# Kernel optimization log

Hardware: AMD Instinct MI355X
Metric: run time of the kernel (lower is better)

## Reference

```python
import jax, jax.numpy as jnp
import numpy as np

N_ROW, N_COL, RANK = 8192, 8192, 256

def setup_inputs() -> dict:
    key = jax.random.key(0)
    k1, k2, k3 = jax.random.split(key, 3)
    X = jax.random.normal(k1, (N_ROW, RANK), dtype=jnp.float32)
    Y = jax.random.normal(k2, (RANK, N_COL), dtype=jnp.float32)
    beta = jax.random.normal(k3, (1,), dtype=jnp.float32)
    return {"X": X, "Y": Y, "beta": beta}

def reference(X, Y, beta):
    # mathematically equal to torch.norm(X[:,None] - Y.T, dim=-1).
    x2 = jnp.sum(X * X, axis=1, keepdims=True)          # (n_row, 1)
    y2 = jnp.sum(Y * Y, axis=0, keepdims=True)          # (1, n_col)
    cross = X @ Y                                        # (n_row, n_col) GEMM
    d2 = jnp.maximum(x2 + y2 - 2.0 * cross, 0.0)
    norms = jnp.sqrt(d2)
    z = -norms + beta                                    # beta broadcasts (1,)
    return z
```

## Files before the change

kernel.cpp:

```cpp
#include <hip/hip_runtime.h>

#define NROW 8192
#define NCOL 8192
#define RANK 256

#define BM 128
#define BN 128
#define BK 64
#define NKT (RANK / BK)

typedef __bf16  bf16x8 __attribute__((ext_vector_type(8)));
typedef float   f32x4  __attribute__((ext_vector_type(4)));

__device__ __forceinline__ unsigned short f2bf(float f) {
    unsigned int u = __builtin_bit_cast(unsigned int, f);
    u += 0x7fffu + ((u >> 16) & 1u);
    return (unsigned short)(u >> 16);
}

__global__ __launch_bounds__(256) void prep_x(const float* __restrict__ X,
                                              unsigned short* __restrict__ Xb,
                                              float* __restrict__ x2) {
    const int row  = blockIdx.x * 4 + (threadIdx.x >> 6);
    const int lane = threadIdx.x & 63;
    const float4 v = ((const float4*)(X + (size_t)row * RANK))[lane];
    float s = v.x * v.x + v.y * v.y + v.z * v.z + v.w * v.w;
    ushort4 b;
    b.x = f2bf(v.x); b.y = f2bf(v.y); b.z = f2bf(v.z); b.w = f2bf(v.w);
    ((ushort4*)(Xb + (size_t)row * RANK))[lane] = b;
    #pragma unroll
    for (int off = 32; off > 0; off >>= 1) s += __shfl_down(s, off);
    if (lane == 0) x2[row] = s;
}

__global__ __launch_bounds__(256) void prep_y(const float* __restrict__ Y,
                                              unsigned short* __restrict__ Ybt,
                                              float* __restrict__ y2) {
    __shared__ float tile[64][65];
    __shared__ float part[256];
    const int t  = threadIdx.x;
    const int j0 = blockIdx.x * 64;
    const int tq = t >> 6;
    const int tl = t & 63;
    float acc = 0.f;
    for (int c = 0; c < 4; ++c) {
        const int k0 = c * 64;
        #pragma unroll
        for (int i = 0; i < 16; ++i) {
            const int kk = tq * 16 + i;
            const float v = Y[(size_t)(k0 + kk) * NCOL + j0 + tl];
            tile[kk][tl] = v;
            acc += v * v;
        }
        __syncthreads();
        #pragma unroll
        for (int i = 0; i < 16; ++i) {
            const int jj = tq * 16 + i;
            Ybt[(size_t)(j0 + jj) * RANK + k0 + tl] = f2bf(tile[tl][jj]);
        }
        __syncthreads();
    }
    part[t] = acc;
    __syncthreads();
    if (t < 64)
        y2[j0 + t] = part[t] + part[t + 64] + part[t + 128] + part[t + 192];
}

__global__ __launch_bounds__(256, 2)
void l2_gemm(const unsigned short* __restrict__ A,
             const unsigned short* __restrict__ Bt,
             const float* __restrict__ x2,
             const float* __restrict__ y2,
             const float* __restrict__ beta_p,
             float* __restrict__ out) {
    __shared__ alignas(16) unsigned short As[2][BM * BK];
    __shared__ alignas(16) unsigned short Bs[2][BN * BK];

    const int t    = threadIdx.x;
    const int wid  = t >> 6;
    const int lane = t & 63;

    const int bid  = blockIdx.x;
    const int xcd  = bid & 7;
    const int seq  = bid >> 3;
    const int ct   = xcd * 8 + (seq & 7);
    const int rt   = seq >> 3;
    const int rowBase = rt * BM;
    const int colBase = ct * BN;

    const int waveM = (wid >> 1) * 64;
    const int waveN = (wid & 1) * 64;

    f32x4 acc[4][4] = {};

    const int lrow = lane >> 3;
    const int lcol = (lane & 7) * 8;

    const unsigned short* gA = A  + (size_t)(rowBase + wid * 8 + lrow) * RANK + lcol;
    const unsigned short* gB = Bt + (size_t)(colBase + wid * 8 + lrow) * RANK + lcol;

    auto stage = [&](int buf, int kt) {
        #pragma unroll
        for (int r = 0; r < 4; ++r) {
            const int rrel = r * 32 + wid * 8;
            __builtin_amdgcn_global_load_lds(
                (__attribute__((address_space(1))) void*)(gA + (size_t)r * 32 * RANK + kt),
                (__attribute__((address_space(3))) void*)(&As[buf][rrel * BK]), 16, 0, 0);
            __builtin_amdgcn_global_load_lds(
                (__attribute__((address_space(1))) void*)(gB + (size_t)r * 32 * RANK + kt),
                (__attribute__((address_space(3))) void*)(&Bs[buf][rrel * BK]), 16, 0, 0);
        }
    };

    auto compute = [&](int buf) {
        #pragma unroll
        for (int ks = 0; ks < BK; ks += 32) {
            const int kfrag = ks + (lane >> 4) * 8;
            bf16x8 af[4], bfr[4];
            #pragma unroll
            for (int mt = 0; mt < 4; ++mt)
                af[mt] = *(const bf16x8*)(&As[buf][(waveM + mt * 16 + (lane & 15)) * BK + kfrag]);
            #pragma unroll
            for (int nt = 0; nt < 4; ++nt)
                bfr[nt] = *(const bf16x8*)(&Bs[buf][(waveN + nt * 16 + (lane & 15)) * BK + kfrag]);
            #pragma unroll
            for (int mt = 0; mt < 4; ++mt)
                #pragma unroll
                for (int nt = 0; nt < 4; ++nt)
                    acc[mt][nt] = __builtin_amdgcn_mfma_f32_16x16x32_bf16(
                        bfr[nt], af[mt], acc[mt][nt], 0, 0, 0);
        }
    };

    stage(0, 0);
    __syncthreads();
    #pragma unroll
    for (int kt = 1; kt < NKT; ++kt) {
        stage(kt & 1, kt * BK);
        compute((kt - 1) & 1);
        __syncthreads();
    }

    const int r0 = rowBase + waveM + (lane & 15);
    const int c0 = colBase + waveN + ((lane >> 4) << 2);
    const float beta = *beta_p;
    float xv[4];
    f32x4 y4[4];
    #pragma unroll
    for (int mt = 0; mt < 4; ++mt) xv[mt] = x2[r0 + mt * 16];
    #pragma unroll
    for (int nt = 0; nt < 4; ++nt) y4[nt] = *(const f32x4*)(y2 + c0 + nt * 16);

    compute((NKT - 1) & 1);

    #pragma unroll
    for (int mt = 0; mt < 4; ++mt) {
        const int row = r0 + mt * 16;
        float* op = out + (size_t)row * NCOL + c0;
        #pragma unroll
        for (int nt = 0; nt < 4; ++nt) {
            const f32x4 a = acc[mt][nt];
            f32x4 z;
            #pragma unroll
            for (int r = 0; r < 4; ++r) {
                float d2 = xv[mt] + y4[nt][r] - 2.0f * a[r];
                z[r] = beta - __builtin_amdgcn_sqrtf(fmaxf(d2, 0.0f));
            }
            __builtin_nontemporal_store(z, (f32x4*)(op + nt * 16));
        }
    }
}

extern "C" void kernel_launch(void* const* d_in, const int* in_sizes, int n_in,
                              void* d_out, int out_size, void* d_ws, size_t ws_size,
                              hipStream_t stream) {
    const float* X    = (const float*)d_in[0];
    const float* Y    = (const float*)d_in[1];
    const float* beta = (const float*)d_in[2];
    float* out = (float*)d_out;

    char* ws = (char*)d_ws;
    unsigned short* Xb  = (unsigned short*)(ws);
    unsigned short* Ybt = (unsigned short*)(ws + (size_t)4 * 1024 * 1024);
    float* x2 = (float*)(ws + (size_t)8 * 1024 * 1024);
    float* y2 = (float*)(ws + (size_t)8 * 1024 * 1024 + 32 * 1024);

    prep_x<<<NROW / 4, 256, 0, stream>>>(X, Xb, x2);
    prep_y<<<NCOL / 64, 256, 0, stream>>>(Y, Ybt, y2);

    l2_gemm<<<dim3(4096), 256, 0, stream>>>(Xb, Ybt, x2, y2, beta, out);
}
```

Baseline: 326.3 us.

## Stage full-K B tile in swizzled LDS, load A fragments directly from global

Replaces the double-buffered K-tiled LDS pipeline with one upfront load of the whole 128x256 B tile into LDS, using an XOR swizzle to avoid bank conflicts. The A operand fragments are now read straight from global memory into registers per k-group, and there is only a single barrier. This removes the per-iteration barriers and the LDS round trip for A. In exchange, A reads are per-lane 16-byte gathers from global memory that depend on cache hits, and nothing overlaps the global B load with compute.

```diff
diff --git a/kernel.cpp b/kernel.cpp
--- a/kernel.cpp
+++ b/kernel.cpp
@@ -6,8 +6,6 @@
 
 #define BM 128
 #define BN 128
-#define BK 64
-#define NKT (RANK / BK)
 
 typedef __bf16  bf16x8 __attribute__((ext_vector_type(8)));
 typedef float   f32x4  __attribute__((ext_vector_type(4)));
@@ -73,8 +71,7 @@
              const float* __restrict__ y2,
              const float* __restrict__ beta_p,
              float* __restrict__ out) {
-    __shared__ alignas(16) unsigned short As[2][BM * BK];
-    __shared__ alignas(16) unsigned short Bs[2][BN * BK];
+    __shared__ alignas(16) unsigned short Bs[BN * RANK];
 
     const int t    = threadIdx.x;
     const int wid  = t >> 6;
@@ -93,56 +90,31 @@
 
     f32x4 acc[4][4] = {};
 
-    const int lrow = lane >> 3;
-    const int lcol = (lane & 7) * 8;
-
-    const unsigned short* gA = A  + (size_t)(rowBase + wid * 8 + lrow) * RANK + lcol;
-    const unsigned short* gB = Bt + (size_t)(colBase + wid * 8 + lrow) * RANK + lcol;
-
-    auto stage = [&](int buf, int kt) {
+    {
+        const int l5 = lane >> 5;
+        const int ls = lane & 31;
         #pragma unroll
-        for (int r = 0; r < 4; ++r) {
-            const int rrel = r * 32 + wid * 8;
+        for (int r = 0; r < 16; ++r) {
+            const int ro = wid * 32 + r * 2 + l5;
+            const int cs = ls ^ (ro & 7);
+            const unsigned short* gp =
+                Bt + (size_t)(colBase + ro) * RANK + cs * 8;
+            unsigned short* lp = &Bs[(wid * 32 + r * 2) * RANK];
             __builtin_amdgcn_global_load_lds(
-                (__attribute__((address_space(1))) void*)(gA + (size_t)r * 32 * RANK + kt),
-                (__attribute__((address_space(3))) void*)(&As[buf][rrel * BK]), 16, 0, 0);
-            __builtin_amdgcn_global_load_lds(
-                (__attribute__((address_space(1))) void*)(gB + (size_t)r * 32 * RANK + kt),
-                (__attribute__((address_space(3))) void*)(&Bs[buf][rrel * BK]), 16, 0, 0);
+                (__attribute__((address_space(1))) void*)gp,
+                (__attribute__((address_space(3))) void*)lp, 16, 0, 0);
         }
-    };
-
-    auto compute = [&](int buf) {
-        #pragma unroll
-        for (int ks = 0; ks < BK; ks += 32) {
-            const int kfrag = ks + (lane >> 4) * 8;
-            bf16x8 af[4], bfr[4];
-            #pragma unroll
-            for (int mt = 0; mt < 4; ++mt)
-                af[mt] = *(const bf16x8*)(&As[buf][(waveM + mt * 16 + (lane & 15)) * BK + kfrag]);
-            #pragma unroll
-            for (int nt = 0; nt < 4; ++nt)
-                bfr[nt] = *(const bf16x8*)(&Bs[buf][(waveN + nt * 16 + (lane & 15)) * BK + kfrag]);
-            #pragma unroll
-            for (int mt = 0; mt < 4; ++mt)
-                #pragma unroll
-                for (int nt = 0; nt < 4; ++nt)
-                    acc[mt][nt] = __builtin_amdgcn_mfma_f32_16x16x32_bf16(
-                        bfr[nt], af[mt], acc[mt][nt], 0, 0, 0);
-        }
-    };
-
-    stage(0, 0);
-    __syncthreads();
-    #pragma unroll
-    for (int kt = 1; kt < NKT; ++kt) {
-        stage(kt & 1, kt * BK);
-        compute((kt - 1) & 1);
-        __syncthreads();
     }
 
     const int r0 = rowBase + waveM + (lane & 15);
     const int c0 = colBase + waveN + ((lane >> 4) << 2);
+    const int koff = (lane >> 4) * 8;
+
+    bf16x8 af0[4];
+    #pragma unroll
+    for (int mt = 0; mt < 4; ++mt)
+        af0[mt] = *(const bf16x8*)(A + (size_t)(r0 + mt * 16) * RANK + koff);
+
     const float beta = *beta_p;
     float xv[4];
     f32x4 y4[4];
@@ -151,7 +123,34 @@
     #pragma unroll
     for (int nt = 0; nt < 4; ++nt) y4[nt] = *(const f32x4*)(y2 + c0 + nt * 16);
 
-    compute((NKT - 1) & 1);
+    __syncthreads();
+
+    #pragma unroll
+    for (int kg = 0; kg < 8; ++kg) {
+        bf16x8 af[4], bfr[4];
+        if (kg == 0) {
+            #pragma unroll
+            for (int mt = 0; mt < 4; ++mt) af[mt] = af0[mt];
+        } else {
+            const int ko = kg * 32 + koff;
+            #pragma unroll
+            for (int mt = 0; mt < 4; ++mt)
+                af[mt] = *(const bf16x8*)(A + (size_t)(r0 + mt * 16) * RANK + ko);
+        }
+        const int sbase = kg * 4 + (lane >> 4);
+        #pragma unroll
+        for (int nt = 0; nt < 4; ++nt) {
+            const int rr = waveN + nt * 16 + (lane & 15);
+            const int s  = sbase ^ (rr & 7);
+            bfr[nt] = *(const bf16x8*)(&Bs[rr * RANK + s * 8]);
+        }
+        #pragma unroll
+        for (int mt = 0; mt < 4; ++mt)
+            #pragma unroll
+            for (int nt = 0; nt < 4; ++nt)
+                acc[mt][nt] = __builtin_amdgcn_mfma_f32_16x16x32_bf16(
+                    bfr[nt], af[mt], acc[mt][nt], 0, 0, 0);
+    }
 
     #pragma unroll
     for (int mt = 0; mt < 4; ++mt) {
```

Result: slower. 350.9 us (+7.5%).

## Stage GEMM epilogue through swizzled LDS for coalesced row stores; simplify grid mapping

Applied to the files above, without the earlier changes.

The epilogue now writes results into a shared-memory tile using an XOR swizzle, then reads them back so that each half-wave stores a full 512-byte contiguous row segment to global memory. The goal is better-coalesced writes of the 256 MB output, which is the dominant cost. The XCD-aware block remapping is replaced by a plain 2D grid, and nontemporal stores become regular stores. This adds two barriers and an LDS round trip, and may lose L2 locality across XCDs.

```diff
diff --git a/kernel.cpp b/kernel.cpp
--- a/kernel.cpp
+++ b/kernel.cpp
@@ -73,20 +73,16 @@
              const float* __restrict__ y2,
              const float* __restrict__ beta_p,
              float* __restrict__ out) {
-    __shared__ alignas(16) unsigned short As[2][BM * BK];
-    __shared__ alignas(16) unsigned short Bs[2][BN * BK];
+    __shared__ alignas(16) unsigned char smem[64 * 1024];
+    auto As = (unsigned short (*)[BM * BK])(smem);
+    auto Bs = (unsigned short (*)[BN * BK])(smem + 32768);
+    float* Cs = (float*)smem;
 
     const int t    = threadIdx.x;
     const int wid  = t >> 6;
     const int lane = t & 63;
-
-    const int bid  = blockIdx.x;
-    const int xcd  = bid & 7;
-    const int seq  = bid >> 3;
-    const int ct   = xcd * 8 + (seq & 7);
-    const int rt   = seq >> 3;
-    const int rowBase = rt * BM;
-    const int colBase = ct * BN;
+    const int rowBase = blockIdx.x * BM;
+    const int colBase = blockIdx.y * BN;
 
     const int waveM = (wid >> 1) * 64;
     const int waveN = (wid & 1) * 64;
@@ -152,11 +148,11 @@
     for (int nt = 0; nt < 4; ++nt) y4[nt] = *(const f32x4*)(y2 + c0 + nt * 16);
 
     compute((NKT - 1) & 1);
+    __syncthreads();
 
     #pragma unroll
     for (int mt = 0; mt < 4; ++mt) {
-        const int row = r0 + mt * 16;
-        float* op = out + (size_t)row * NCOL + c0;
+        const int trow = waveM + mt * 16 + (lane & 15);
         #pragma unroll
         for (int nt = 0; nt < 4; ++nt) {
             const f32x4 a = acc[mt][nt];
@@ -166,7 +162,21 @@
                 float d2 = xv[mt] + y4[nt][r] - 2.0f * a[r];
                 z[r] = beta - __builtin_amdgcn_sqrtf(fmaxf(d2, 0.0f));
             }
-            __builtin_nontemporal_store(z, (f32x4*)(op + nt * 16));
+            const int slot = ((waveN >> 2) + nt * 4 + (lane >> 4)) ^ (trow & 7);
+            *(f32x4*)(&Cs[trow * 128 + slot * 4]) = z;
+        }
+    }
+    __syncthreads();
+
+    {
+        const int l5 = lane >> 5;
+        const int g  = lane & 31;
+        #pragma unroll
+        for (int i = 0; i < 16; ++i) {
+            const int trow = wid * 32 + i * 2 + l5;
+            const int slot = g ^ (trow & 7);
+            const f32x4 v = *(const f32x4*)(&Cs[trow * 128 + slot * 4]);
+            *(f32x4*)(out + (size_t)(rowBase + trow) * NCOL + colBase + g * 4) = v;
         }
     }
 }
@@ -188,5 +198,6 @@
     prep_x<<<NROW / 4, 256, 0, stream>>>(X, Xb, x2);
     prep_y<<<NCOL / 64, 256, 0, stream>>>(Y, Ybt, y2);
 
-    l2_gemm<<<dim3(4096), 256, 0, stream>>>(Xb, Ybt, x2, y2, beta, out);
-}
+    dim3 grid(NROW / BM, NCOL / BN);
+    l2_gemm<<<grid, 256, 0, stream>>>(Xb, Ybt, x2, y2, beta, out);
+}
```

Measured after the change: 308.2 us. 5.5% less time.
